# Kernel optimization log

Measured on AMD Instinct MI355X. Metric: run time of the kernel, lower is better.

The kernel has to match this reference:

```python
import jax, jax.numpy as jnp
import numpy as np

NQ = 10          # qubits per register
DIM = 2 ** NQ    # 1024 amplitudes
N_CLS = 10       # canonical images (one per class)
N = 16384        # batch of samples
IMG = 28 * 28    # 784 pixels, zero-padded to DIM


def setup_inputs() -> dict:
    key = jax.random.key(0)
    k1, k2, k3 = jax.random.split(key, 3)
    z_re = jax.random.normal(k1, (N, DIM), dtype=jnp.float32)
    z_im = jax.random.normal(k2, (N, DIM), dtype=jnp.float32)
    # inputs are quantum states -> L2-normalize the complex vectors
    nrm = jnp.sqrt(jnp.sum(z_re * z_re + z_im * z_im, axis=1, keepdims=True))
    z_re = z_re / nrm
    z_im = z_im / nrm
    canon = jax.random.uniform(k3, (N_CLS, 1, 28, 28), dtype=jnp.float32)
    return {"z_re": z_re, "z_im": z_im, "canon": canon}


def reference(z_re, z_im, canon):
    # reshape_norm_padding: flatten, zero-pad to 2^nq, L2-normalize (real amplitudes)
    ref = canon.reshape(N_CLS, IMG)
    ref = jnp.pad(ref, ((0, 0), (0, DIM - IMG)))                  # [C, DIM]
    ref = ref / jnp.linalg.norm(ref, axis=1, keepdims=True)
    # Swap test: <Z_anc> = |<val|ref>|^2. ref is real, so with val = z_re + i*z_im:
    #   <val|ref> = (z_re @ ref^T) - i*(z_im @ ref^T)
    s_re = jnp.einsum('nd,cd->nc', z_re, ref)                     # [N, C]
    s_im = jnp.einsum('nd,cd->nc', z_im, ref)                     # [N, C]
    return s_re * s_re + s_im * s_im                              # [N, C] float32
```

## Files before the change

kernel.cpp:

```cpp
#include <hip/hip_runtime.h>

#define DIM    1024
#define N_CLS  10
#define NB     16
#define NROWS  16384
#define IMG    784
#define K_HALF 512
#define CHUNKS 16

typedef __attribute__((ext_vector_type(8))) short sh8;
typedef __attribute__((ext_vector_type(4))) float f4;

__device__ __forceinline__ unsigned f2bf2(float lo, float hi) {
  unsigned a = __float_as_uint(lo);
  unsigned b = __float_as_uint(hi);
  a += 0x7FFFu + ((a >> 16) & 1u);
  b += 0x7FFFu + ((b >> 16) & 1u);
  return (a >> 16) | (b & 0xFFFF0000u);
}

__device__ __forceinline__ unsigned short f2bf(float x) {
  unsigned a = __float_as_uint(x);
  a += 0x7FFFu + ((a >> 16) & 1u);
  return (unsigned short)(a >> 16);
}

__device__ __forceinline__ sh8 pack8(f4 v0, f4 v1) {
  union {
    unsigned u[4];
    sh8 s;
  } r;
  r.u[0] = f2bf2(v0.x, v0.y);
  r.u[1] = f2bf2(v0.z, v0.w);
  r.u[2] = f2bf2(v1.x, v1.y);
  r.u[3] = f2bf2(v1.z, v1.w);
  return r.s;
}

__global__ void ref_prep_kernel(const float* __restrict__ canon,
                                unsigned short* __restrict__ refb) {
  __shared__ float red[256];
  const int c = blockIdx.x;
  const int t = threadIdx.x;

  float inv = 0.f;
  if (c < N_CLS) {
    const float* src = canon + c * IMG;
    float ss = 0.f;
    for (int d = t; d < IMG; d += 256) {
      float v = src[d];
      ss += v * v;
    }
    red[t] = ss;
    __syncthreads();
    for (int s = 128; s > 0; s >>= 1) {
      if (t < s) red[t] += red[t + s];
      __syncthreads();
    }
    inv = 1.0f / sqrtf(red[0]);
  }

  for (int d = t; d < DIM; d += 256) {
    float v = (c < N_CLS && d < IMG) ? canon[c * IMG + d] * inv : 0.f;
    refb[c * DIM + d] = f2bf(v);
  }
}

__global__ __launch_bounds__(256, 2) void swaptest_kernel(
    const float* __restrict__ zre, const float* __restrict__ zim,
    const unsigned short* __restrict__ refb, float* __restrict__ out) {
  __shared__ float part[8][2][64];

  const int tid  = threadIdx.x;
  const int lane = tid & 63;
  const int wv   = tid >> 6;
  const int st   = wv >> 1;
  const int kh   = wv & 1;
  const int mrow = lane & 15;
  const int kq   = lane >> 4;

  const int row   = blockIdx.x * 32 + st * 16 + mrow;
  const int kbase = kh * K_HALF + kq * 8;

  sh8 bfrag[CHUNKS];
#pragma unroll
  for (int i = 0; i < CHUNKS; ++i)
    bfrag[i] = *(const sh8*)&refb[mrow * DIM + kbase + i * 32];

  const float* pre = zre + (size_t)row * DIM + kbase;
  const float* pim = zim + (size_t)row * DIM + kbase;

  f4 accre = {0.f, 0.f, 0.f, 0.f};
  f4 accim = {0.f, 0.f, 0.f, 0.f};

  f4 cre0 = *(const f4*)(pre);
  f4 cre1 = *(const f4*)(pre + 4);
  f4 cim0 = *(const f4*)(pim);
  f4 cim1 = *(const f4*)(pim + 4);
#pragma unroll
  for (int i = 0; i < CHUNKS; ++i) {
    f4 nre0, nre1, nim0, nim1;
    if (i + 1 < CHUNKS) {
      nre0 = *(const f4*)(pre + (i + 1) * 32);
      nre1 = *(const f4*)(pre + (i + 1) * 32 + 4);
      nim0 = *(const f4*)(pim + (i + 1) * 32);
      nim1 = *(const f4*)(pim + (i + 1) * 32 + 4);
    }
    const sh8 a_re = pack8(cre0, cre1);
    const sh8 a_im = pack8(cim0, cim1);
    accre = __builtin_amdgcn_mfma_f32_16x16x32_bf16(a_re, bfrag[i], accre,
                                                    0, 0, 0);
    accim = __builtin_amdgcn_mfma_f32_16x16x32_bf16(a_im, bfrag[i], accim,
                                                    0, 0, 0);
    if (i + 1 < CHUNKS) {
      cre0 = nre0; cre1 = nre1;
      cim0 = nim0; cim1 = nim1;
    }
  }

  if (kh == 1) {
#pragma unroll
    for (int r = 0; r < 4; ++r) {
      part[r][st][lane]     = accre[r];
      part[4 + r][st][lane] = accim[r];
    }
  }
  __syncthreads();

  if (kh == 0 && mrow < N_CLS) {
    const int orow0 = blockIdx.x * 32 + st * 16 + kq * 4;
#pragma unroll
    for (int r = 0; r < 4; ++r) {
      const float re = accre[r] + part[r][st][lane];
      const float im = accim[r] + part[4 + r][st][lane];
      out[(size_t)(orow0 + r) * N_CLS + mrow] = re * re + im * im;
    }
  }
}

extern "C" void kernel_launch(void* const* d_in, const int* in_sizes, int n_in,
                              void* d_out, int out_size, void* d_ws,
                              size_t ws_size, hipStream_t stream) {
  const float* z_re = (const float*)d_in[0];
  const float* z_im = (const float*)d_in[1];
  const float* canon = (const float*)d_in[2];
  float* out = (float*)d_out;
  unsigned short* refb = (unsigned short*)d_ws;

  ref_prep_kernel<<<NB, 256, 0, stream>>>(canon, refb);

  const int nblk = NROWS / 32;
  swaptest_kernel<<<nblk, 256, 0, stream>>>(z_re, z_im, refb, out);
}
```

Baseline: 152.4 us.

## Split K across eight waves per 16-row block with LDS reduction

Each block now handles 16 rows with 8 waves, each wave covering a 128-wide K slice (4 MFMA chunks) instead of 2 waves per 16 rows over 512-wide halves. The partial sums from all 8 waves are reduced through shared memory and one thread per output element writes the result. This gives more blocks and more waves in flight to hide the memory latency of streaming z_re/z_im. It drops the explicit software prefetch and adds an 8-way LDS reduction and a barrier per block.

```diff
diff --git a/kernel.cpp b/kernel.cpp
--- a/kernel.cpp
+++ b/kernel.cpp
@@ -5,8 +5,9 @@
 #define NB     16
 #define NROWS  16384
 #define IMG    784
-#define K_HALF 512
-#define CHUNKS 16
+#define KSPLIT 8
+#define KW     128
+#define CHUNKS 4
 
 typedef __attribute__((ext_vector_type(8))) short sh8;
 typedef __attribute__((ext_vector_type(4))) float f4;
@@ -66,21 +67,19 @@
   }
 }
 
-__global__ __launch_bounds__(256, 2) void swaptest_kernel(
+__global__ __launch_bounds__(512, 8) void swaptest_kernel(
     const float* __restrict__ zre, const float* __restrict__ zim,
     const unsigned short* __restrict__ refb, float* __restrict__ out) {
-  __shared__ float part[8][2][64];
+  __shared__ float part[KSPLIT][64][9];
 
   const int tid  = threadIdx.x;
   const int lane = tid & 63;
   const int wv   = tid >> 6;
-  const int st   = wv >> 1;
-  const int kh   = wv & 1;
   const int mrow = lane & 15;
   const int kq   = lane >> 4;
 
-  const int row   = blockIdx.x * 32 + st * 16 + mrow;
-  const int kbase = kh * K_HALF + kq * 8;
+  const int row   = blockIdx.x * 16 + mrow;
+  const int kbase = wv * KW + kq * 8;
 
   sh8 bfrag[CHUNKS];
 #pragma unroll
@@ -93,48 +92,37 @@
   f4 accre = {0.f, 0.f, 0.f, 0.f};
   f4 accim = {0.f, 0.f, 0.f, 0.f};
 
-  f4 cre0 = *(const f4*)(pre);
-  f4 cre1 = *(const f4*)(pre + 4);
-  f4 cim0 = *(const f4*)(pim);
-  f4 cim1 = *(const f4*)(pim + 4);
 #pragma unroll
   for (int i = 0; i < CHUNKS; ++i) {
-    f4 nre0, nre1, nim0, nim1;
-    if (i + 1 < CHUNKS) {
-      nre0 = *(const f4*)(pre + (i + 1) * 32);
-      nre1 = *(const f4*)(pre + (i + 1) * 32 + 4);
-      nim0 = *(const f4*)(pim + (i + 1) * 32);
-      nim1 = *(const f4*)(pim + (i + 1) * 32 + 4);
-    }
-    const sh8 a_re = pack8(cre0, cre1);
-    const sh8 a_im = pack8(cim0, cim1);
-    accre = __builtin_amdgcn_mfma_f32_16x16x32_bf16(a_re, bfrag[i], accre,
-                                                    0, 0, 0);
-    accim = __builtin_amdgcn_mfma_f32_16x16x32_bf16(a_im, bfrag[i], accim,
-                                                    0, 0, 0);
-    if (i + 1 < CHUNKS) {
-      cre0 = nre0; cre1 = nre1;
-      cim0 = nim0; cim1 = nim1;
-    }
+    const f4 cre0 = *(const f4*)(pre + i * 32);
+    const f4 cre1 = *(const f4*)(pre + i * 32 + 4);
+    const f4 cim0 = *(const f4*)(pim + i * 32);
+    const f4 cim1 = *(const f4*)(pim + i * 32 + 4);
+    accre = __builtin_amdgcn_mfma_f32_16x16x32_bf16(pack8(cre0, cre1),
+                                                    bfrag[i], accre, 0, 0, 0);
+    accim = __builtin_amdgcn_mfma_f32_16x16x32_bf16(pack8(cim0, cim1),
+                                                    bfrag[i], accim, 0, 0, 0);
   }
 
-  if (kh == 1) {
 #pragma unroll
-    for (int r = 0; r < 4; ++r) {
-      part[r][st][lane]     = accre[r];
-      part[4 + r][st][lane] = accim[r];
-    }
+  for (int r = 0; r < 4; ++r) {
+    part[wv][lane][r]     = accre[r];
+    part[wv][lane][4 + r] = accim[r];
   }
   __syncthreads();
 
-  if (kh == 0 && mrow < N_CLS) {
-    const int orow0 = blockIdx.x * 32 + st * 16 + kq * 4;
+  if (tid < 16 * N_CLS) {
+    const int r = tid / N_CLS;
+    const int c = tid - r * N_CLS;
+    const int pl = ((r >> 2) << 4) | c;
+    const int reg = r & 3;
+    float are = 0.f, aim = 0.f;
 #pragma unroll
-    for (int r = 0; r < 4; ++r) {
-      const float re = accre[r] + part[r][st][lane];
-      const float im = accim[r] + part[4 + r][st][lane];
-      out[(size_t)(orow0 + r) * N_CLS + mrow] = re * re + im * im;
+    for (int w = 0; w < KSPLIT; ++w) {
+      are += part[w][pl][reg];
+      aim += part[w][pl][4 + reg];
     }
+    out[(size_t)(blockIdx.x * 16 + r) * N_CLS + c] = are * are + aim * aim;
   }
 }
 
@@ -149,6 +137,6 @@
 
   ref_prep_kernel<<<NB, 256, 0, stream>>>(canon, refb);
 
-  const int nblk = NROWS / 32;
-  swaptest_kernel<<<nblk, 256, 0, stream>>>(z_re, z_im, refb, out);
+  const int nblk = NROWS / 16;
+  swaptest_kernel<<<nblk, 512, 0, stream>>>(z_re, z_im, refb, out);
 }
```

New measurement: 154.7 us. No clear change (+1.5%).
